# Optimization experiments

Measured on AMD Instinct MI355X. Metric: run time of the kernel, lower is better.

Reference implementation:

```python
import jax, jax.numpy as jnp
import numpy as np

DIM = 512
NUM_HEADS = 8
HEAD_DIM = DIM // NUM_HEADS
SCALE = HEAD_DIM ** -0.5


def setup_inputs() -> dict:
    key = jax.random.key(0)
    k1, k2, k3, k4 = jax.random.split(key, 4)
    x = jax.random.normal(k1, (2, 4096, DIM), dtype=jnp.float32)
    # Linear weights stored as (in, out) for x @ W; torch Linear(dim, 3*dim, bias=False)
    w_qkv = jax.random.normal(k2, (DIM, 3 * DIM), dtype=jnp.float32) * (DIM ** -0.5)
    w_proj = jax.random.normal(k3, (DIM, DIM), dtype=jnp.float32) * (DIM ** -0.5)
    b_proj = jax.random.normal(k4, (DIM,), dtype=jnp.float32) * 0.02
    return {"x": x, "w_qkv": w_qkv, "w_proj": w_proj, "b_proj": b_proj}


def reference(x, w_qkv, w_proj, b_proj):
    B, N, C = x.shape
    qkv = (x @ w_qkv).reshape(B, N, 3, NUM_HEADS, HEAD_DIM)
    qkv = jnp.transpose(qkv, (2, 0, 3, 1, 4))  # (3, B, H, N, hd)
    q, k, v = qkv[0], qkv[1], qkv[2]
    attn = jnp.einsum("bhnd,bhmd->bhnm", q, k) * SCALE
    attn = jax.nn.softmax(attn, axis=-1)
    out = jnp.einsum("bhnm,bhmd->bhnd", attn, v)
    out = jnp.transpose(out, (0, 2, 1, 3)).reshape(B, N, C)
    return out @ w_proj + b_proj
```

## Files before the change

kernel.cpp:

```cpp
#include <hip/hip_runtime.h>
#include <hip/hip_bf16.h>
#include <stdint.h>
#include <math.h>

#define NC3 1536
#define QSCALE 0.18033688011111907f
#define KSPLIT 2

typedef __attribute__((ext_vector_type(8))) short short8;
typedef __attribute__((ext_vector_type(4))) short short4v;
typedef __attribute__((ext_vector_type(4))) float f32x4;
typedef __attribute__((ext_vector_type(16))) float f32x16;

static __device__ __forceinline__ short f2bf(float f) {
    union { __hip_bfloat16 h; short s; } u;
    u.h = __float2bfloat16(f);
    return u.s;
}
static __device__ __forceinline__ float bf2f(short s) {
    return __uint_as_float(((unsigned)(unsigned short)s) << 16);
}
static __device__ __forceinline__ unsigned bfpack(float a, float b) {
    unsigned ua = (__float_as_uint(a) + 0x8000u) >> 16;
    unsigned ub = (__float_as_uint(b) + 0x8000u) & 0xffff0000u;
    return ua | ub;
}

#define GLD_LDS(g, l)                                                          \
    __builtin_amdgcn_global_load_lds(                                          \
        (const __attribute__((address_space(1))) void*)(g),                    \
        (__attribute__((address_space(3))) void*)(l), 16, 0, 0)

__global__ __launch_bounds__(256) void cast_f32_bf16(const float* __restrict__ src,
                                                     short* __restrict__ dst, int n4) {
    int i = blockIdx.x * 256 + threadIdx.x;
    if (i < n4) {
        float4 v = ((const float4*)src)[i];
        short4v o = {f2bf(v.x), f2bf(v.y), f2bf(v.z), f2bf(v.w)};
        ((short4v*)dst)[i] = o;
    }
}

__global__ __launch_bounds__(256) void transpose_f32_bf16(const float* __restrict__ src,
                                                          short* __restrict__ dst,
                                                          int R, int C) {
    __shared__ short t[32][33];
    int c0 = blockIdx.x * 32, r0 = blockIdx.y * 32;
    int tx = threadIdx.x, ty = threadIdx.y;
#pragma unroll
    for (int i = 0; i < 4; i++)
        t[ty + i * 8][tx] = f2bf(src[(size_t)(r0 + ty + i * 8) * C + c0 + tx]);
    __syncthreads();
#pragma unroll
    for (int i = 0; i < 4; i++)
        dst[(size_t)(c0 + ty + i * 8) * R + r0 + tx] = t[tx][ty + i * 8];
}

__global__ __launch_bounds__(256) void transpose_v(const short* __restrict__ QKV,
                                                   short* __restrict__ VT) {
    __shared__ short t[32][33];
    int n0 = blockIdx.x * 32, d0 = blockIdx.y * 32;
    int bh = blockIdx.z;
    int b = bh >> 3, h = bh & 7;
    const short* src = QKV + (size_t)b * 4096 * NC3 + 1024 + h * 64;
    short* dst = VT + (size_t)bh * 64 * 4096;
    int tx = threadIdx.x, ty = threadIdx.y;
#pragma unroll
    for (int i = 0; i < 4; i++)
        t[ty + i * 8][tx] = src[(size_t)(n0 + ty + i * 8) * NC3 + d0 + tx];
    __syncthreads();
#pragma unroll
    for (int i = 0; i < 4; i++)
        dst[(size_t)(d0 + ty + i * 8) * 4096 + n0 + tx] = t[tx][ty + i * 8];
}

__global__ __launch_bounds__(256) void combine_partials(const short* __restrict__ Op0,
                                                        const short* __restrict__ Op1,
                                                        const float* __restrict__ lp,
                                                        short* __restrict__ AO) {
    int i = (blockIdx.x * 256 + threadIdx.x) * 8;
    int row = i >> 9;
    int h = (i >> 6) & 7;
    float linv = 1.0f / (lp[row * 8 + h] + lp[65536 + row * 8 + h]);
    short8 a = *(const short8*)(Op0 + i);
    short8 b = *(const short8*)(Op1 + i);
    short8 o;
#pragma unroll
    for (int j = 0; j < 8; j++)
        o[j] = f2bf((bf2f(a[j]) + bf2f(b[j])) * linv);
    *(short8*)(AO + i) = o;
}

template <int NMODE>
__global__ __launch_bounds__(256) void gemm128(const short* __restrict__ A,
                                               const short* __restrict__ Bt,
                                               short* __restrict__ OutB,
                                               float* __restrict__ OutF,
                                               const float* __restrict__ bias) {
    __shared__ __attribute__((aligned(16))) short a_sm[128 * 64];
    __shared__ __attribute__((aligned(16))) short b_sm[128 * 64];
    const int tid = threadIdx.x;
    const int lane = tid & 63;
    const int wave = tid >> 6;
    const int wr = wave >> 1, wc = wave & 1;
    const int quad = lane >> 4;
    const int l15 = lane & 15;
    const int m0 = blockIdx.x * 128;
    const int n0 = blockIdx.y * 128;
    const int srow = lane >> 3;
    const int schunk = (lane & 7) ^ srow;

    f32x4 zero4 = {0.f, 0.f, 0.f, 0.f};
    f32x4 acc[4][4];
#pragma unroll
    for (int i = 0; i < 4; i++)
#pragma unroll
        for (int j = 0; j < 4; j++) acc[i][j] = zero4;

    for (int k0 = 0; k0 < 512; k0 += 64) {
        __syncthreads();
#pragma unroll
        for (int i = 0; i < 4; i++) {
            int r0 = wave * 32 + i * 8;
            const short* ga = A + (size_t)(m0 + r0 + srow) * 512 + k0 + schunk * 8;
            GLD_LDS(ga, a_sm + r0 * 64);
            const short* gb = Bt + (size_t)(n0 + r0 + srow) * 512 + k0 + schunk * 8;
            GLD_LDS(gb, b_sm + r0 * 64);
        }
        __syncthreads();
#pragma unroll
        for (int kk = 0; kk < 2; kk++) {
            short8 af[4], bfr[4];
#pragma unroll
            for (int mi = 0; mi < 4; mi++) {
                int row = wr * 64 + mi * 16 + l15;
                int slot = (kk * 4 + quad) ^ (row & 7);
                af[mi] = *(const short8*)(a_sm + row * 64 + slot * 8);
            }
#pragma unroll
            for (int ni = 0; ni < 4; ni++) {
                int row = wc * 64 + ni * 16 + l15;
                int slot = (kk * 4 + quad) ^ (row & 7);
                bfr[ni] = *(const short8*)(b_sm + row * 64 + slot * 8);
            }
#pragma unroll
            for (int mi = 0; mi < 4; mi++)
#pragma unroll
                for (int ni = 0; ni < 4; ni++)
                    acc[mi][ni] = __builtin_amdgcn_mfma_f32_16x16x32_bf16(
                        af[mi], bfr[ni], acc[mi][ni], 0, 0, 0);
        }
    }

#pragma unroll
    for (int mi = 0; mi < 4; mi++) {
#pragma unroll
        for (int ni = 0; ni < 4; ni++) {
            int gm0 = m0 + wr * 64 + mi * 16 + quad * 4;
            int gn = n0 + wc * 64 + ni * 16 + l15;
            f32x4 v = acc[mi][ni];
#pragma unroll
            for (int r = 0; r < 4; r++) {
                int gm = gm0 + r;
                float val = v[r];
                if (NMODE == 0) {
                    float o = (gn < 512) ? val * QSCALE : val;
                    OutB[(size_t)gm * NC3 + gn] = f2bf(o);
                } else {
                    OutF[(size_t)gm * 512 + gn] = val + bias[gn];
                }
            }
        }
    }
}

__global__ __launch_bounds__(256, 4) void attn_kernel(const short* __restrict__ QKV,
                                                      const short* __restrict__ VT,
                                                      short* __restrict__ Op0,
                                                      short* __restrict__ Op1,
                                                      float* __restrict__ lpart) {
    __shared__ __attribute__((aligned(16))) short k_sm[2][64 * 64];
    __shared__ __attribute__((aligned(16))) short v_sm[2][64 * 64];

    const int tid = threadIdx.x;
    const int lane = tid & 63;
    const int wave = tid >> 6;
    const int l31 = lane & 31;
    const int hi = lane >> 5;
    const int qt = blockIdx.x;
    const int bh = blockIdx.y;
    const int ks = blockIdx.z;
    const int b = bh >> 3, h = bh & 7;
    const size_t tokbase = (size_t)b * 4096;
    const int rowbase = qt * 128;
    const int kt0 = ks * (64 / KSPLIT);
    const int kt1 = kt0 + (64 / KSPLIT);
    const short* Qg = QKV + h * 64;
    const short* Kg = QKV + 512 + h * 64;
    const short* VTg = VT + (size_t)bh * 64 * 4096;
    const int srow = lane >> 3;
    const int schunk = (lane & 7) ^ srow;

    short* qstage = &k_sm[0][0];
#pragma unroll
    for (int i = 0; i < 4; i++) {
        int r0 = wave * 32 + i * 8;
        GLD_LDS(Qg + (tokbase + rowbase + r0 + srow) * NC3 + schunk * 8, qstage + r0 * 64);
    }
    __syncthreads();
    const int qrow = wave * 32 + l31;
    short8 qf[4];
#pragma unroll
    for (int kk = 0; kk < 4; kk++) {
        int slot = (kk * 2 + hi) ^ (qrow & 7);
        qf[kk] = *(const short8*)(qstage + qrow * 64 + slot * 8);
    }
    __syncthreads();

#pragma unroll
    for (int i = 0; i < 2; i++) {
        int r0 = wave * 16 + i * 8;
        GLD_LDS(Kg + (tokbase + (size_t)kt0 * 64 + r0 + srow) * NC3 + schunk * 8,
                k_sm[0] + r0 * 64);
        GLD_LDS(VTg + (size_t)(r0 + srow) * 4096 + kt0 * 64 + schunk * 8,
                v_sm[0] + r0 * 64);
    }

    const short onebf = (short)0x3F80;
    const short8 ones = {onebf, onebf, onebf, onebf, onebf, onebf, onebf, onebf};

    f32x16 acc_o[2], acc_l;
#pragma unroll
    for (int i = 0; i < 16; i++) { acc_o[0][i] = 0.f; acc_o[1][i] = 0.f; acc_l[i] = 0.f; }

    for (int kt = kt0; kt < kt1; kt++) {
        __syncthreads();
        const int cur = kt & 1;
        if (kt < kt1 - 1) {
            const int nb = cur ^ 1;
#pragma unroll
            for (int i = 0; i < 2; i++) {
                int r0 = wave * 16 + i * 8;
                GLD_LDS(Kg + (tokbase + (size_t)(kt + 1) * 64 + r0 + srow) * NC3 + schunk * 8,
                        k_sm[nb] + r0 * 64);
                GLD_LDS(VTg + (size_t)(r0 + srow) * 4096 + (kt + 1) * 64 + schunk * 8,
                        v_sm[nb] + r0 * 64);
            }
        }

        f32x16 s[2];
#pragma unroll
        for (int i = 0; i < 16; i++) { s[0][i] = 0.f; s[1][i] = 0.f; }
#pragma unroll
        for (int kk = 0; kk < 4; kk++) {
#pragma unroll
            for (int kb = 0; kb < 2; kb++) {
                int row = kb * 32 + l31;
                int slot = (kk * 2 + hi) ^ (row & 7);
                short8 kf = *(const short8*)(k_sm[cur] + row * 64 + slot * 8);
                s[kb] = __builtin_amdgcn_mfma_f32_32x32x16_bf16(kf, qf[kk], s[kb], 0, 0, 0);
            }
        }

        unsigned pk[2][8];
#pragma unroll
        for (int kb = 0; kb < 2; kb++)
#pragma unroll
            for (int i = 0; i < 16; i += 2)
                pk[kb][i >> 1] = bfpack(__builtin_amdgcn_exp2f(s[kb][i]),
                                        __builtin_amdgcn_exp2f(s[kb][i + 1]));

        short8 pf[4];
#pragma unroll
        for (int kb = 0; kb < 2; kb++) {
#pragma unroll
            for (int f = 0; f < 2; f++) {
                unsigned b0 = pk[kb][4 * f + 0], b1 = pk[kb][4 * f + 1];
                unsigned b2 = pk[kb][4 * f + 2], b3 = pk[kb][4 * f + 3];
                unsigned s0 = hi ? b0 : b2;
                unsigned s1 = hi ? b1 : b3;
                unsigned t0 = (unsigned)__shfl_xor((int)s0, 32, 64);
                unsigned t1 = (unsigned)__shfl_xor((int)s1, 32, 64);
                union { unsigned u[4]; short8 s8; } cv;
                cv.u[0] = hi ? t0 : b0;
                cv.u[1] = hi ? t1 : b1;
                cv.u[2] = hi ? b2 : t0;
                cv.u[3] = hi ? b3 : t1;
                pf[kb * 2 + f] = cv.s8;
            }
        }

#pragma unroll
        for (int g = 0; g < 4; g++) {
            acc_l = __builtin_amdgcn_mfma_f32_32x32x16_bf16(ones, pf[g], acc_l, 0, 0, 0);
#pragma unroll
            for (int db = 0; db < 2; db++) {
                int row = db * 32 + l31;
                int slot = (g * 2 + hi) ^ (row & 7);
                short8 vf = *(const short8*)(v_sm[cur] + row * 64 + slot * 8);
                acc_o[db] = __builtin_amdgcn_mfma_f32_32x32x16_bf16(vf, pf[g], acc_o[db], 0, 0, 0);
            }
        }
    }

    __syncthreads();

    size_t growq = tokbase + rowbase + qrow;
    if (hi == 0) lpart[(size_t)ks * 65536 + growq * 8 + h] = acc_l[0];

    short* osm = &k_sm[0][0] + wave * 2048;
#pragma unroll
    for (int db = 0; db < 2; db++) {
#pragma unroll
        for (int i = 0; i < 16; i += 2) {
            int d = db * 32 + (i & 3) + 8 * (i >> 2) + 4 * hi;
            unsigned pkd = bfpack(acc_o[db][i], acc_o[db][i + 1]);
            int slot = (d >> 3) ^ (l31 & 7);
            *(unsigned*)(osm + l31 * 64 + slot * 8 + (d & 7)) = pkd;
        }
    }
    short* Od = (ks == 0) ? Op0 : Op1;
#pragma unroll
    for (int j = 0; j < 4; j++) {
        int r = lane >> 1;
        int c = (lane & 1) * 4 + j;
        int slot = c ^ (r & 7);
        short8 ov = *(const short8*)(osm + r * 64 + slot * 8);
        size_t grow = tokbase + rowbase + wave * 32 + r;
        *(short8*)(Od + grow * 512 + h * 64 + c * 8) = ov;
    }
}

extern "C" void kernel_launch(void* const* d_in, const int* in_sizes, int n_in,
                              void* d_out, int out_size, void* d_ws, size_t ws_size,
                              hipStream_t stream) {
    (void)in_sizes; (void)n_in; (void)out_size; (void)ws_size;
    const float* x = (const float*)d_in[0];
    const float* wqkv = (const float*)d_in[1];
    const float* wproj = (const float*)d_in[2];
    const float* bproj = (const float*)d_in[3];
    float* out = (float*)d_out;

    short* ws = (short*)d_ws;
    short* xbf = ws;
    short* wqkvT = xbf + (size_t)4194304;
    short* wprojT = wqkvT + (size_t)1536 * 512;
    short* QKV = wprojT + (size_t)512 * 512;
    short* VTb = QKV + (size_t)8192 * 1536;
    short* AO = VTb + (size_t)16 * 64 * 4096;
    short* Opart1 = xbf;
    float* lpart = (float*)wqkvT;

    cast_f32_bf16<<<4096, 256, 0, stream>>>(x, xbf, 1048576);
    transpose_f32_bf16<<<dim3(48, 16), dim3(32, 8), 0, stream>>>(wqkv, wqkvT, 512, 1536);
    transpose_f32_bf16<<<dim3(16, 16), dim3(32, 8), 0, stream>>>(wproj, wprojT, 512, 512);
    gemm128<0><<<dim3(64, 12), 256, 0, stream>>>(xbf, wqkvT, QKV, nullptr, nullptr);
    transpose_v<<<dim3(128, 2, 16), dim3(32, 8), 0, stream>>>(QKV, VTb);
    attn_kernel<<<dim3(32, 16, KSPLIT), 256, 0, stream>>>(QKV, VTb, AO, Opart1, lpart);
    combine_partials<<<2048, 256, 0, stream>>>(AO, Opart1, lpart, AO);
    gemm128<1><<<dim3(64, 4), 256, 0, stream>>>(AO, wprojT, nullptr, out, bproj);
}
```

Baseline: 219.8 us.

## Use fp16 P·V MFMA with permuted V layout, fuse weight transposes, narrow proj tiles

```diff
diff --git a/kernel.cpp b/kernel.cpp
--- a/kernel.cpp
+++ b/kernel.cpp
@@ -11,6 +11,8 @@
 typedef __attribute__((ext_vector_type(4))) short short4v;
 typedef __attribute__((ext_vector_type(4))) float f32x4;
 typedef __attribute__((ext_vector_type(16))) float f32x16;
+typedef __attribute__((ext_vector_type(8))) _Float16 f16x8;
+typedef __attribute__((ext_vector_type(2))) __fp16 fp16x2;
 
 static __device__ __forceinline__ short f2bf(float f) {
     union { __hip_bfloat16 h; short s; } u;
@@ -24,6 +26,11 @@
     unsigned ua = (__float_as_uint(a) + 0x8000u) >> 16;
     unsigned ub = (__float_as_uint(b) + 0x8000u) & 0xffff0000u;
     return ua | ub;
+}
+static __device__ __forceinline__ unsigned hpack(float a, float b) {
+    union { fp16x2 h; unsigned u; } c;
+    c.h = __builtin_amdgcn_cvt_pkrtz(a, b);
+    return c.u;
 }
 
 #define GLD_LDS(g, l)                                                          \
@@ -41,9 +48,16 @@
     }
 }
 
-__global__ __launch_bounds__(256) void transpose_f32_bf16(const float* __restrict__ src,
-                                                          short* __restrict__ dst,
-                                                          int R, int C) {
+__global__ __launch_bounds__(256) void transpose_weights(const float* __restrict__ wqkv,
+                                                         short* __restrict__ wqkvT,
+                                                         const float* __restrict__ wproj,
+                                                         short* __restrict__ wprojT) {
+    const float* src;
+    short* dst;
+    int C;
+    if (blockIdx.z == 0) { src = wqkv; dst = wqkvT; C = 1536; }
+    else                 { if (blockIdx.x >= 16) return; src = wproj; dst = wprojT; C = 512; }
+    const int R = 512;
     __shared__ short t[32][33];
     int c0 = blockIdx.x * 32, r0 = blockIdx.y * 32;
     int tx = threadIdx.x, ty = threadIdx.y;
@@ -69,9 +83,13 @@
     for (int i = 0; i < 4; i++)
         t[ty + i * 8][tx] = src[(size_t)(n0 + ty + i * 8) * NC3 + d0 + tx];
     __syncthreads();
-#pragma unroll
-    for (int i = 0; i < 4; i++)
-        dst[(size_t)(d0 + ty + i * 8) * 4096 + n0 + tx] = t[tx][ty + i * 8];
+    int ptx = (tx & ~12) | ((tx & 4) << 1) | ((tx & 8) >> 1);
+#pragma unroll
+    for (int i = 0; i < 4; i++) {
+        union { __fp16 h; short s; } cv;
+        cv.h = (__fp16)bf2f(t[tx][ty + i * 8]);
+        dst[(size_t)(d0 + ty + i * 8) * 4096 + n0 + ptx] = cv.s;
+    }
 }
 
 __global__ __launch_bounds__(256) void combine_partials(const short* __restrict__ Op0,
@@ -91,14 +109,15 @@
     *(short8*)(AO + i) = o;
 }
 
-template <int NMODE>
+template <int NMODE, int NTILE>
 __global__ __launch_bounds__(256) void gemm128(const short* __restrict__ A,
                                                const short* __restrict__ Bt,
                                                short* __restrict__ OutB,
                                                float* __restrict__ OutF,
                                                const float* __restrict__ bias) {
+    constexpr int NI = NTILE / 32;
     __shared__ __attribute__((aligned(16))) short a_sm[128 * 64];
-    __shared__ __attribute__((aligned(16))) short b_sm[128 * 64];
+    __shared__ __attribute__((aligned(16))) short b_sm[NTILE * 64];
     const int tid = threadIdx.x;
     const int lane = tid & 63;
     const int wave = tid >> 6;
@@ -106,16 +125,16 @@
     const int quad = lane >> 4;
     const int l15 = lane & 15;
     const int m0 = blockIdx.x * 128;
-    const int n0 = blockIdx.y * 128;
+    const int n0 = blockIdx.y * NTILE;
     const int srow = lane >> 3;
     const int schunk = (lane & 7) ^ srow;
 
     f32x4 zero4 = {0.f, 0.f, 0.f, 0.f};
-    f32x4 acc[4][4];
+    f32x4 acc[4][NI];
 #pragma unroll
     for (int i = 0; i < 4; i++)
 #pragma unroll
-        for (int j = 0; j < 4; j++) acc[i][j] = zero4;
+        for (int j = 0; j < NI; j++) acc[i][j] = zero4;
 
     for (int k0 = 0; k0 < 512; k0 += 64) {
         __syncthreads();
@@ -124,13 +143,17 @@
             int r0 = wave * 32 + i * 8;
             const short* ga = A + (size_t)(m0 + r0 + srow) * 512 + k0 + schunk * 8;
             GLD_LDS(ga, a_sm + r0 * 64);
+        }
+#pragma unroll
+        for (int i = 0; i < NTILE / 32; i++) {
+            int r0 = wave * (NTILE / 4) + i * 8;
             const short* gb = Bt + (size_t)(n0 + r0 + srow) * 512 + k0 + schunk * 8;
             GLD_LDS(gb, b_sm + r0 * 64);
         }
         __syncthreads();
 #pragma unroll
         for (int kk = 0; kk < 2; kk++) {
-            short8 af[4], bfr[4];
+            short8 af[4], bfr[NI];
 #pragma unroll
             for (int mi = 0; mi < 4; mi++) {
                 int row = wr * 64 + mi * 16 + l15;
@@ -138,15 +161,15 @@
                 af[mi] = *(const short8*)(a_sm + row * 64 + slot * 8);
             }
 #pragma unroll
-            for (int ni = 0; ni < 4; ni++) {
-                int row = wc * 64 + ni * 16 + l15;
+            for (int ni = 0; ni < NI; ni++) {
+                int row = wc * (NTILE / 2) + ni * 16 + l15;
                 int slot = (kk * 4 + quad) ^ (row & 7);
                 bfr[ni] = *(const short8*)(b_sm + row * 64 + slot * 8);
             }
 #pragma unroll
             for (int mi = 0; mi < 4; mi++)
 #pragma unroll
-                for (int ni = 0; ni < 4; ni++)
+                for (int ni = 0; ni < NI; ni++)
                     acc[mi][ni] = __builtin_amdgcn_mfma_f32_16x16x32_bf16(
                         af[mi], bfr[ni], acc[mi][ni], 0, 0, 0);
         }
@@ -155,9 +178,9 @@
 #pragma unroll
     for (int mi = 0; mi < 4; mi++) {
 #pragma unroll
-        for (int ni = 0; ni < 4; ni++) {
+        for (int ni = 0; ni < NI; ni++) {
             int gm0 = m0 + wr * 64 + mi * 16 + quad * 4;
-            int gn = n0 + wc * 64 + ni * 16 + l15;
+            int gn = n0 + wc * (NTILE / 2) + ni * 16 + l15;
             f32x4 v = acc[mi][ni];
 #pragma unroll
             for (int r = 0; r < 4; r++) {
@@ -226,8 +249,8 @@
                 v_sm[0] + r0 * 64);
     }
 
-    const short onebf = (short)0x3F80;
-    const short8 ones = {onebf, onebf, onebf, onebf, onebf, onebf, onebf, onebf};
+    const _Float16 onef = (_Float16)1.0f;
+    const f16x8 ones16 = {onef, onef, onef, onef, onef, onef, onef, onef};
 
     f32x16 acc_o[2], acc_l;
 #pragma unroll
@@ -267,38 +290,21 @@
         for (int kb = 0; kb < 2; kb++)
 #pragma unroll
             for (int i = 0; i < 16; i += 2)
-                pk[kb][i >> 1] = bfpack(__builtin_amdgcn_exp2f(s[kb][i]),
-                                        __builtin_amdgcn_exp2f(s[kb][i + 1]));
-
-        short8 pf[4];
-#pragma unroll
-        for (int kb = 0; kb < 2; kb++) {
-#pragma unroll
-            for (int f = 0; f < 2; f++) {
-                unsigned b0 = pk[kb][4 * f + 0], b1 = pk[kb][4 * f + 1];
-                unsigned b2 = pk[kb][4 * f + 2], b3 = pk[kb][4 * f + 3];
-                unsigned s0 = hi ? b0 : b2;
-                unsigned s1 = hi ? b1 : b3;
-                unsigned t0 = (unsigned)__shfl_xor((int)s0, 32, 64);
-                unsigned t1 = (unsigned)__shfl_xor((int)s1, 32, 64);
-                union { unsigned u[4]; short8 s8; } cv;
-                cv.u[0] = hi ? t0 : b0;
-                cv.u[1] = hi ? t1 : b1;
-                cv.u[2] = hi ? b2 : t0;
-                cv.u[3] = hi ? b3 : t1;
-                pf[kb * 2 + f] = cv.s8;
-            }
-        }
+                pk[kb][i >> 1] = hpack(__builtin_amdgcn_exp2f(s[kb][i]),
+                                       __builtin_amdgcn_exp2f(s[kb][i + 1]));
 
 #pragma unroll
         for (int g = 0; g < 4; g++) {
-            acc_l = __builtin_amdgcn_mfma_f32_32x32x16_bf16(ones, pf[g], acc_l, 0, 0, 0);
+            union { unsigned u[4]; f16x8 v; } pf;
+#pragma unroll
+            for (int t = 0; t < 4; t++) pf.u[t] = pk[g >> 1][4 * (g & 1) + t];
+            acc_l = __builtin_amdgcn_mfma_f32_32x32x16_f16(ones16, pf.v, acc_l, 0, 0, 0);
 #pragma unroll
             for (int db = 0; db < 2; db++) {
                 int row = db * 32 + l31;
                 int slot = (g * 2 + hi) ^ (row & 7);
-                short8 vf = *(const short8*)(v_sm[cur] + row * 64 + slot * 8);
-                acc_o[db] = __builtin_amdgcn_mfma_f32_32x32x16_bf16(vf, pf[g], acc_o[db], 0, 0, 0);
+                f16x8 vf = *(const f16x8*)(v_sm[cur] + row * 64 + slot * 8);
+                acc_o[db] = __builtin_amdgcn_mfma_f32_32x32x16_f16(vf, pf.v, acc_o[db], 0, 0, 0);
             }
         }
     }
@@ -352,11 +358,10 @@
     float* lpart = (float*)wqkvT;
 
     cast_f32_bf16<<<4096, 256, 0, stream>>>(x, xbf, 1048576);
-    transpose_f32_bf16<<<dim3(48, 16), dim3(32, 8), 0, stream>>>(wqkv, wqkvT, 512, 1536);
-    transpose_f32_bf16<<<dim3(16, 16), dim3(32, 8), 0, stream>>>(wproj, wprojT, 512, 512);
-    gemm128<0><<<dim3(64, 12), 256, 0, stream>>>(xbf, wqkvT, QKV, nullptr, nullptr);
+    transpose_weights<<<dim3(48, 16, 2), dim3(32, 8), 0, stream>>>(wqkv, wqkvT, wproj, wprojT);
+    gemm128<0, 128><<<dim3(64, 12), 256, 0, stream>>>(xbf, wqkvT, QKV, nullptr, nullptr);
     transpose_v<<<dim3(128, 2, 16), dim3(32, 8), 0, stream>>>(QKV, VTb);
     attn_kernel<<<dim3(32, 16, KSPLIT), 256, 0, stream>>>(QKV, VTb, AO, Opart1, lpart);
     combine_partials<<<2048, 256, 0, stream>>>(AO, Opart1, lpart, AO);
-    gemm128<1><<<dim3(64, 4), 256, 0, stream>>>(AO, wprojT, nullptr, out, bproj);
-}
+    gemm128<1, 64><<<dim3(64, 8), 256, 0, stream>>>(AO, wprojT, nullptr, out, bproj);
+}
```

New measurement: 203.2 us. -7.5%, faster.
